# Performance work log

Measured on AMD Instinct MI355X. Metric: run time of the kernel, lower is better.

Reference implementation:

```python
import jax, jax.numpy as jnp
import numpy as np

N = 100000
E = 1600000
D_IN = 128
D_H = 128


def setup_inputs() -> dict:
    key = jax.random.key(0)
    ks = jax.random.split(key, 8)
    x = jax.random.normal(ks[0], (N, D_IN), dtype=jnp.float32)
    edge_index = jax.random.randint(ks[1], (2, E), 0, N, dtype=jnp.int64)
    edge_weights = jax.random.uniform(ks[2], (E,), dtype=jnp.float32)
    # GCNConv params (glorot-ish scale), bias zeros like PyG default init reset
    W1 = jax.random.normal(ks[3], (D_IN, D_H), dtype=jnp.float32) / np.sqrt(D_IN)
    b1 = jnp.zeros((D_H,), dtype=jnp.float32)
    W2 = jax.random.normal(ks[4], (D_H, D_H), dtype=jnp.float32) / np.sqrt(D_H)
    b2 = jnp.zeros((D_H,), dtype=jnp.float32)
    a_prelu = jnp.full((D_H,), 0.25, dtype=jnp.float32)  # nn.PReLU(hidden_dim)
    return {"x": x, "edge_index": edge_index, "edge_weights": edge_weights,
            "W1": W1, "b1": b1, "W2": W2, "b2": b2, "a_prelu": a_prelu}


def _gcn_norm(edge_index, edge_weights, n_nodes):
    # add self loops (weight 1), symmetric normalization deg^-1/2 A deg^-1/2
    loop = jnp.arange(n_nodes, dtype=edge_index.dtype)
    src = jnp.concatenate([edge_index[0], loop])
    dst = jnp.concatenate([edge_index[1], loop])
    w = jnp.concatenate([edge_weights, jnp.ones((n_nodes,), edge_weights.dtype)])
    deg = jax.ops.segment_sum(w, dst, num_segments=n_nodes)
    dis = jnp.where(deg > 0, jax.lax.rsqrt(jnp.maximum(deg, 1e-12)), 0.0)
    norm = dis[src] * w * dis[dst]
    return src, dst, norm


def _gcn_layer(h, W, b, src, dst, norm, n_nodes):
    h = h @ W                                   # [N, D] linear (no bias)
    msg = h[src] * norm[:, None]                # gather + scale  [E+N, D]
    out = jax.ops.segment_sum(msg, dst, num_segments=n_nodes)
    return out + b


def _prelu(z, a):
    return jnp.where(z >= 0, z, a * z)


def reference(x, edge_index, edge_weights, W1, b1, W2, b2, a_prelu):
    n = x.shape[0]
    src, dst, norm = _gcn_norm(edge_index, edge_weights, n)
    z = _prelu(_gcn_layer(x, W1, b1, src, dst, norm, n), a_prelu)
    z = _prelu(_gcn_layer(z, W2, b2, src, dst, norm, n), a_prelu)
    return z
```

## Files before the change

kernel.cpp:

```cpp
#include <hip/hip_runtime.h>
#include <hip/hip_fp16.h>

#define D 128
#define CAP 64
#define NBKT 512
#define CHUNK 4096
#define BKTCAP 5120

typedef _Float16 f16x8 __attribute__((ext_vector_type(8)));
typedef float f32x4 __attribute__((ext_vector_type(4)));

__global__ __launch_bounds__(256) void k_bin(const int* __restrict__ ei,
        const float* __restrict__ ew, int* __restrict__ gcur,
        int2* __restrict__ gbkt, int e, int nbin,
        const float* __restrict__ W1, const float* __restrict__ W2,
        __half* __restrict__ Wpk1, __half* __restrict__ Wpk2) {
    if (blockIdx.x >= nbin) {
        int gidx = (blockIdx.x - nbin) * 256 + threadIdx.x;
        if (gidx >= 4096) return;
        const float* W = (gidx < 2048) ? W1 : W2;
        __half* P = (gidx < 2048) ? Wpk1 : Wpk2;
        int idx = gidx & 2047;
        int lane = idx & 63, nt = (idx >> 6) & 7, ks = idx >> 9;
        int col = nt * 16 + (lane & 15);
        int kb = ks * 32 + (lane >> 4) * 8;
        #pragma unroll
        for (int j = 0; j < 8; ++j)
            P[idx * 8 + j] = __float2half(W[(kb + j) * D + col]);
        return;
    }
    __shared__ int hist[NBKT];
    __shared__ int base[NBKT];
    int t = threadIdx.x;
    int b0 = blockIdx.x * CHUNK;
    int cnt = min(CHUNK, e - b0);
    for (int i = t; i < NBKT; i += 256) hist[i] = 0;
    __syncthreads();
    int meta[16]; float w[16]; int pos[16]; int bkt[16];
    #pragma unroll
    for (int j = 0; j < 16; ++j) {
        int li = t + j * 256;
        bkt[j] = -1;
        if (li < cnt) {
            int i = b0 + li;
            int d = ei[e + i];
            int s = ei[i];
            bkt[j] = d >> 8;
            meta[j] = s | ((d & 255) << 24);
            w[j] = ew[i];
            pos[j] = atomicAdd(&hist[bkt[j]], 1);
        }
    }
    __syncthreads();
    for (int i = t; i < NBKT; i += 256)
        if (hist[i] > 0) base[i] = atomicAdd(&gcur[i], hist[i]);
    __syncthreads();
    #pragma unroll
    for (int j = 0; j < 16; ++j) {
        if (bkt[j] >= 0) {
            int idx = base[bkt[j]] + pos[j];
            if (idx < BKTCAP)
                gbkt[(size_t)bkt[j] * BKTCAP + idx] =
                    make_int2(meta[j], __float_as_int(w[j]));
        }
    }
}

__global__ __launch_bounds__(1024) void k_scat2(const int2* __restrict__ gbkt,
        const int* __restrict__ gcur, const float2* __restrict__ X,
        int2* __restrict__ slot, int* __restrict__ rsc, float* __restrict__ dis,
        __half2* __restrict__ xh, int n) {
    __shared__ int cur[256];
    __shared__ float wsum[256];
    __shared__ float disv[256];
    int bkt = blockIdx.x;
    int nodebase = bkt << 8;
    int t = threadIdx.x;
    int cnt = min(gcur[bkt], BKTCAP);
    if (t < 256) { cur[t] = 0; wsum[t] = 0.f; }
    __syncthreads();
    for (int i = t; i < cnt; i += 1024) {
        int2 r = gbkt[(size_t)bkt * BKTCAP + i];
        int dl = (unsigned)r.x >> 24;
        int pos = atomicAdd(&cur[dl], 1);
        atomicAdd(&wsum[dl], __int_as_float(r.y));
        if (pos < CAP)
            slot[(((size_t)(nodebase + dl)) << 6) + pos] =
                make_int2(r.x & 0xFFFFFF, r.y);
    }
    __syncthreads();
    if (t < 256) {
        int v = nodebase + t;
        float dv = 1.f;
        if (v < n) {
            dv = rsqrtf(1.0f + wsum[t]);
            dis[v] = dv;
            rsc[v] = cur[t];
        }
        disv[t] = dv;
    }
    __syncthreads();
    int nrow = min(256, n - nodebase);
    size_t rowbase = (size_t)nodebase << 6;
    for (int idx = t; idx < nrow * 64; idx += 1024) {
        float dv2 = disv[idx >> 6];
        float2 f = X[rowbase + idx];
        xh[rowbase + idx] = __floats2half2_rn(dv2 * f.x, dv2 * f.y);
    }
}

template <int NU>
__device__ __forceinline__ void aggbatch(int j0, int eslot, int dg, int voff,
        float wf, const char* __restrict__ Hc, float (&acc)[8]) {
    int vo[NU]; float w[NU];
    #pragma unroll
    for (int u = 0; u < NU; ++u) {
        int sl = j0 + 4 * u + eslot;
        vo[u] = __shfl(voff, sl);
        w[u] = __shfl(wf, sl);
    }
    f16x8 g[NU];
    #pragma unroll
    for (int u = 0; u < NU; ++u)
        g[u] = *(const f16x8*)(Hc + vo[u] + (dg << 4));
    #pragma unroll
    for (int u = 0; u < NU; ++u) {
        #pragma unroll
        for (int d = 0; d < 8; ++d)
            acc[d] = fmaf(w[u], (float)g[u][d], acc[d]);
    }
}

__global__ __launch_bounds__(256) void k_agg(const __half2* __restrict__ Hs,
        const int2* __restrict__ slot, const int* __restrict__ rsc,
        const float* __restrict__ dis, __half2* __restrict__ out, int n) {
    int wid = threadIdx.x >> 6, lane = threadIdx.x & 63;
    int v = blockIdx.x * 4 + wid;
    if (v >= n) return;
    int eslot = lane >> 4;
    int dg = lane & 15;
    int c = min(rsc[v], 62);
    int c1 = c + 1;
    const int2* row = slot + ((size_t)v << 6);
    const char* Hc = (const char*)Hs;

    int2 mm;
    if (lane == 0) mm = make_int2(v, 0x3f800000);
    else if (lane < c1) mm = row[lane - 1];
    else mm = make_int2(v, 0);
    int voff = mm.x << 8;
    float wf = __int_as_float(mm.y);

    float acc[8];
    #pragma unroll
    for (int d = 0; d < 8; ++d) acc[d] = 0.f;

    int j0 = 0;
    for (; j0 + 16 <= c1; j0 += 16) aggbatch<4>(j0, eslot, dg, voff, wf, Hc, acc);
    for (; j0 < c1; j0 += 8)        aggbatch<2>(j0, eslot, dg, voff, wf, Hc, acc);

    #pragma unroll
    for (int d = 0; d < 8; ++d) {
        acc[d] += __shfl_xor(acc[d], 16);
        acc[d] += __shfl_xor(acc[d], 32);
    }
    if (eslot == 0) {
        float dv = dis[v];
        union { f16x8 v8; __half2 h[4]; } o;
        #pragma unroll
        for (int d = 0; d < 4; ++d)
            o.h[d] = __floats2half2_rn(dv * acc[2 * d], dv * acc[2 * d + 1]);
        *(f16x8*)((char*)out + ((size_t)v << 8) + (dg << 4)) = o.v8;
    }
}

template <bool HALF_OUT>
__global__ __launch_bounds__(256) void k_gemm(const __half* __restrict__ A,
        const __half* __restrict__ Wpk, const float* __restrict__ b,
        const float* __restrict__ ap, const float* __restrict__ dis,
        void* __restrict__ Cv, int n) {
    int t = threadIdx.x;
    int wv = t >> 6, lane = t & 63;
    int base = blockIdx.x * 64 + wv * 16;
    int row = base + (lane & 15);
    int rowc = min(row, n - 1);
    int kg = lane >> 4;

    const f16x8* Arow = (const f16x8*)(A + (size_t)rowc * D);
    f16x8 afr[4];
    #pragma unroll
    for (int ks = 0; ks < 4; ++ks) afr[ks] = Arow[ks * 4 + kg];

    const f16x8* Wp = (const f16x8*)Wpk;
    f32x4 acc[8];
    #pragma unroll
    for (int nt = 0; nt < 8; ++nt) acc[nt] = (f32x4){0.f, 0.f, 0.f, 0.f};

    #pragma unroll
    for (int ks = 0; ks < 4; ++ks) {
        #pragma unroll
        for (int nt = 0; nt < 8; ++nt) {
            f16x8 bfr = Wp[(ks * 8 + nt) * 64 + lane];
            acc[nt] = __builtin_amdgcn_mfma_f32_16x16x32_f16(afr[ks], bfr, acc[nt], 0, 0, 0);
        }
    }

    int c0 = lane & 15;
    int r0 = base + (lane >> 4) * 4;
    float dv[4];
    #pragma unroll
    for (int q = 0; q < 4; ++q)
        dv[q] = HALF_OUT ? dis[min(r0 + q, n - 1)] : 1.0f;
    #pragma unroll
    for (int nt = 0; nt < 8; ++nt) {
        int col = nt * 16 + c0;
        float bb = b[col], aa = ap[col];
        #pragma unroll
        for (int q = 0; q < 4; ++q) {
            int r = r0 + q;
            if (r < n) {
                float z = acc[nt][q] + bb;
                z = (z >= 0.f) ? z : aa * z;
                if (HALF_OUT) ((__half*)Cv)[(size_t)r * D + col] = __float2half(dv[q] * z);
                else          ((float*)Cv)[(size_t)r * D + col] = z;
            }
        }
    }
}


extern "C" void kernel_launch(void* const* d_in, const int* in_sizes, int n_in,
                              void* d_out, int out_size, void* d_ws, size_t ws_size,
                              hipStream_t stream) {
    const float* x  = (const float*)d_in[0];
    const int*   ei = (const int*)d_in[1];
    const float* ew = (const float*)d_in[2];
    const float* W1 = (const float*)d_in[3];
    const float* b1 = (const float*)d_in[4];
    const float* W2 = (const float*)d_in[5];
    const float* b2 = (const float*)d_in[6];
    const float* ap = (const float*)d_in[7];

    int n = in_sizes[0] / D;
    int e = in_sizes[2];

    int*     gcur = (int*)d_ws;
    float*   dis  = (float*)(gcur + NBKT);
    int*     rsc  = (int*)(dis + n);
    int2*    gbkt = (int2*)(rsc + n);
    int2*    slot = gbkt + (size_t)NBKT * BKTCAP;
    __half2* xh   = (__half2*)(slot + (size_t)n * CAP);
    __half2* z1h  = xh + (size_t)n * 64;
    __half2* ah   = z1h + (size_t)n * 64;
    __half*  Wpk1 = (__half*)(ah + (size_t)n * 64);
    __half*  Wpk2 = Wpk1 + 16384;
    float*   out  = (float*)d_out;

    int nbin = (e + CHUNK - 1) / CHUNK;
    int nbb  = (n + 255) / 256;
    int nbw  = (n + 3) / 4;
    int nbg  = (n + 63) / 64;

    hipMemsetAsync(gcur, 0, NBKT * sizeof(int), stream);
    k_bin<<<nbin + 16, 256, 0, stream>>>(ei, ew, gcur, gbkt, e, nbin, W1, W2, Wpk1, Wpk2);
    k_scat2<<<nbb, 1024, 0, stream>>>(gbkt, gcur, (const float2*)x, slot, rsc, dis, xh, n);

    k_agg<<<nbw, 256, 0, stream>>>(xh, slot, rsc, dis, ah, n);
    k_gemm<true><<<nbg, 256, 0, stream>>>((const __half*)ah, Wpk1, b1, ap, dis, (void*)z1h, n);
    k_agg<<<nbw, 256, 0, stream>>>(z1h, slot, rsc, dis, ah, n);
    k_gemm<false><<<nbg, 256, 0, stream>>>((const __half*)ah, Wpk2, b2, ap, dis, (void*)out, n);
}
```

Measured before the change: 226.1 us.

## Slice feature matrices into column panels and pack edge metadata into 32 bits

Intermediate half-precision feature matrices are stored as four 32-column slices, each holding 64 bytes per node. The aggregation kernel is split so each block processes one slice for two node groups, with 16 edges in flight per wave and 4 lanes per row. Edge slots now pack a 17-bit source index and an fp16 weight into one int, which halves metadata traffic. The aim is to make the gathered working set per slice small enough to stay in cache. The cost is fp16 edge weights, a limit of 131072 nodes, and four times as many aggregation blocks each reading the slot rows.

```diff
diff --git a/kernel.cpp b/kernel.cpp
--- a/kernel.cpp
+++ b/kernel.cpp
@@ -68,8 +68,8 @@
 
 __global__ __launch_bounds__(1024) void k_scat2(const int2* __restrict__ gbkt,
         const int* __restrict__ gcur, const float2* __restrict__ X,
-        int2* __restrict__ slot, int* __restrict__ rsc, float* __restrict__ dis,
-        __half2* __restrict__ xh, int n) {
+        int* __restrict__ mslot, int* __restrict__ rsc, float* __restrict__ dis,
+        __half* __restrict__ xh, int n) {
     __shared__ int cur[256];
     __shared__ float wsum[256];
     __shared__ float disv[256];
@@ -83,10 +83,13 @@
         int2 r = gbkt[(size_t)bkt * BKTCAP + i];
         int dl = (unsigned)r.x >> 24;
         int pos = atomicAdd(&cur[dl], 1);
-        atomicAdd(&wsum[dl], __int_as_float(r.y));
-        if (pos < CAP)
-            slot[(((size_t)(nodebase + dl)) << 6) + pos] =
-                make_int2(r.x & 0xFFFFFF, r.y);
+        float w = __int_as_float(r.y);
+        atomicAdd(&wsum[dl], w);
+        if (pos < CAP) {
+            unsigned hb = (unsigned)__half_as_ushort(__float2half(w));
+            mslot[(((size_t)(nodebase + dl)) << 6) + pos] =
+                (r.x & 0x1FFFF) | (int)(hb << 17);
+        }
     }
     __syncthreads();
     if (t < 256) {
@@ -100,77 +103,65 @@
         disv[t] = dv;
     }
     __syncthreads();
+    size_t n32 = (size_t)n * 32;
     int nrow = min(256, n - nodebase);
-    size_t rowbase = (size_t)nodebase << 6;
     for (int idx = t; idx < nrow * 64; idx += 1024) {
-        float dv2 = disv[idx >> 6];
-        float2 f = X[rowbase + idx];
-        xh[rowbase + idx] = __floats2half2_rn(dv2 * f.x, dv2 * f.y);
-    }
-}
-
-template <int NU>
-__device__ __forceinline__ void aggbatch(int j0, int eslot, int dg, int voff,
-        float wf, const char* __restrict__ Hc, float (&acc)[8]) {
-    int vo[NU]; float w[NU];
-    #pragma unroll
-    for (int u = 0; u < NU; ++u) {
-        int sl = j0 + 4 * u + eslot;
-        vo[u] = __shfl(voff, sl);
-        w[u] = __shfl(wf, sl);
-    }
-    f16x8 g[NU];
-    #pragma unroll
-    for (int u = 0; u < NU; ++u)
-        g[u] = *(const f16x8*)(Hc + vo[u] + (dg << 4));
-    #pragma unroll
-    for (int u = 0; u < NU; ++u) {
-        #pragma unroll
-        for (int d = 0; d < 8; ++d)
-            acc[d] = fmaf(w[u], (float)g[u][d], acc[d]);
-    }
-}
-
-__global__ __launch_bounds__(256) void k_agg(const __half2* __restrict__ Hs,
-        const int2* __restrict__ slot, const int* __restrict__ rsc,
-        const float* __restrict__ dis, __half2* __restrict__ out, int n) {
+        int r = idx >> 6, dp = idx & 63;
+        int grow = nodebase + r;
+        float dv2 = disv[r];
+        float2 f = X[((size_t)grow << 6) + dp];
+        __half2 h = __floats2half2_rn(dv2 * f.x, dv2 * f.y);
+        *(__half2*)(xh + (size_t)(dp >> 4) * n32 + (size_t)grow * 32 + ((dp & 15) << 1)) = h;
+    }
+}
+
+__global__ __launch_bounds__(256) void k_agg(const __half* __restrict__ Hs,
+        const int* __restrict__ mslot, const int* __restrict__ rsc,
+        const float* __restrict__ dis, __half* __restrict__ outp, int n) {
+    int sub = blockIdx.x & 7;
+    int slice = sub >> 1;
+    int nodeblock = (blockIdx.x >> 3) * 2 + (sub & 1);
     int wid = threadIdx.x >> 6, lane = threadIdx.x & 63;
-    int v = blockIdx.x * 4 + wid;
+    int v = nodeblock * 4 + wid;
     if (v >= n) return;
-    int eslot = lane >> 4;
-    int dg = lane & 15;
+    int eg = lane >> 2;
+    int quad = lane & 3;
     int c = min(rsc[v], 62);
     int c1 = c + 1;
-    const int2* row = slot + ((size_t)v << 6);
-    const char* Hc = (const char*)Hs;
-
-    int2 mm;
-    if (lane == 0) mm = make_int2(v, 0x3f800000);
-    else if (lane < c1) mm = row[lane - 1];
-    else mm = make_int2(v, 0);
-    int voff = mm.x << 8;
-    float wf = __int_as_float(mm.y);
+    const int* mrow = mslot + ((size_t)v << 6);
+
+    int mm;
+    if (lane == 0) mm = v | (int)(0x3C00u << 17);
+    else if (lane < c1) mm = mrow[lane - 1];
+    else mm = v;
+
+    size_t n32 = (size_t)n * 32;
+    const char* Hb = (const char*)(Hs + (size_t)slice * n32);
 
     float acc[8];
     #pragma unroll
     for (int d = 0; d < 8; ++d) acc[d] = 0.f;
 
-    int j0 = 0;
-    for (; j0 + 16 <= c1; j0 += 16) aggbatch<4>(j0, eslot, dg, voff, wf, Hc, acc);
-    for (; j0 < c1; j0 += 8)        aggbatch<2>(j0, eslot, dg, voff, wf, Hc, acc);
-
-    #pragma unroll
-    for (int d = 0; d < 8; ++d) {
-        acc[d] += __shfl_xor(acc[d], 16);
-        acc[d] += __shfl_xor(acc[d], 32);
-    }
-    if (eslot == 0) {
+    for (int j0 = 0; j0 < c1; j0 += 16) {
+        int mv = __shfl(mm, j0 + eg);
+        int src = mv & 0x1FFFF;
+        float w = __half2float(__ushort_as_half((unsigned short)((unsigned)mv >> 17)));
+        f16x8 g = *(const f16x8*)(Hb + ((size_t)src << 6) + (quad << 4));
+        #pragma unroll
+        for (int d = 0; d < 8; ++d) acc[d] = fmaf(w, (float)g[d], acc[d]);
+    }
+    #pragma unroll
+    for (int off = 4; off <= 32; off <<= 1) {
+        #pragma unroll
+        for (int d = 0; d < 8; ++d) acc[d] += __shfl_xor(acc[d], off);
+    }
+    if (eg == 0) {
         float dv = dis[v];
         union { f16x8 v8; __half2 h[4]; } o;
         #pragma unroll
         for (int d = 0; d < 4; ++d)
             o.h[d] = __floats2half2_rn(dv * acc[2 * d], dv * acc[2 * d + 1]);
-        *(f16x8*)((char*)out + ((size_t)v << 8) + (dg << 4)) = o.v8;
+        *(f16x8*)((char*)(outp + (size_t)slice * n32) + ((size_t)v << 6) + (quad << 4)) = o.v8;
     }
 }
 
@@ -185,11 +176,12 @@
     int row = base + (lane & 15);
     int rowc = min(row, n - 1);
     int kg = lane >> 4;
-
-    const f16x8* Arow = (const f16x8*)(A + (size_t)rowc * D);
+    size_t n32 = (size_t)n * 32;
+
     f16x8 afr[4];
     #pragma unroll
-    for (int ks = 0; ks < 4; ++ks) afr[ks] = Arow[ks * 4 + kg];
+    for (int ks = 0; ks < 4; ++ks)
+        afr[ks] = *(const f16x8*)(A + (size_t)ks * n32 + (size_t)rowc * 32 + kg * 8);
 
     const f16x8* Wp = (const f16x8*)Wpk;
     f32x4 acc[8];
@@ -221,8 +213,12 @@
             if (r < n) {
                 float z = acc[nt][q] + bb;
                 z = (z >= 0.f) ? z : aa * z;
-                if (HALF_OUT) ((__half*)Cv)[(size_t)r * D + col] = __float2half(dv[q] * z);
-                else          ((float*)Cv)[(size_t)r * D + col] = z;
+                if (HALF_OUT) {
+                    ((__half*)Cv)[(size_t)(nt >> 1) * n32 + (size_t)r * 32 +
+                                  ((nt & 1) * 16 + c0)] = __float2half(dv[q] * z);
+                } else {
+                    ((float*)Cv)[(size_t)r * D + col] = z;
+                }
             }
         }
     }
@@ -244,29 +240,30 @@
     int n = in_sizes[0] / D;
     int e = in_sizes[2];
 
-    int*     gcur = (int*)d_ws;
-    float*   dis  = (float*)(gcur + NBKT);
-    int*     rsc  = (int*)(dis + n);
-    int2*    gbkt = (int2*)(rsc + n);
-    int2*    slot = gbkt + (size_t)NBKT * BKTCAP;
-    __half2* xh   = (__half2*)(slot + (size_t)n * CAP);
-    __half2* z1h  = xh + (size_t)n * 64;
-    __half2* ah   = z1h + (size_t)n * 64;
-    __half*  Wpk1 = (__half*)(ah + (size_t)n * 64);
-    __half*  Wpk2 = Wpk1 + 16384;
-    float*   out  = (float*)d_out;
+    int*     gcur  = (int*)d_ws;
+    float*   dis   = (float*)(gcur + NBKT);
+    int*     rsc   = (int*)(dis + n);
+    int2*    gbkt  = (int2*)(rsc + n);
+    int*     mslot = (int*)(gbkt + (size_t)NBKT * BKTCAP);
+    __half*  xh    = (__half*)(mslot + (size_t)n * 64);
+    __half*  z1h   = xh + (size_t)n * 128;
+    __half*  ah    = z1h + (size_t)n * 128;
+    __half*  Wpk1  = ah + (size_t)n * 128;
+    __half*  Wpk2  = Wpk1 + 16384;
+    float*   out   = (float*)d_out;
 
     int nbin = (e + CHUNK - 1) / CHUNK;
     int nbb  = (n + 255) / 256;
-    int nbw  = (n + 3) / 4;
+    int NB   = (n + 3) / 4;
+    int nba  = ((NB + 1) / 2) * 8;
     int nbg  = (n + 63) / 64;
 
     hipMemsetAsync(gcur, 0, NBKT * sizeof(int), stream);
     k_bin<<<nbin + 16, 256, 0, stream>>>(ei, ew, gcur, gbkt, e, nbin, W1, W2, Wpk1, Wpk2);
-    k_scat2<<<nbb, 1024, 0, stream>>>(gbkt, gcur, (const float2*)x, slot, rsc, dis, xh, n);
-
-    k_agg<<<nbw, 256, 0, stream>>>(xh, slot, rsc, dis, ah, n);
-    k_gemm<true><<<nbg, 256, 0, stream>>>((const __half*)ah, Wpk1, b1, ap, dis, (void*)z1h, n);
-    k_agg<<<nbw, 256, 0, stream>>>(z1h, slot, rsc, dis, ah, n);
-    k_gemm<false><<<nbg, 256, 0, stream>>>((const __half*)ah, Wpk2, b2, ap, dis, (void*)out, n);
-}
+    k_scat2<<<nbb, 1024, 0, stream>>>(gbkt, gcur, (const float2*)x, mslot, rsc, dis, xh, n);
+
+    k_agg<<<nba, 256, 0, stream>>>(xh, mslot, rsc, dis, ah, n);
+    k_gemm<true><<<nbg, 256, 0, stream>>>(ah, Wpk1, b1, ap, dis, (void*)z1h, n);
+    k_agg<<<nba, 256, 0, stream>>>(z1h, mslot, rsc, dis, ah, n);
+    k_gemm<false><<<nbg, 256, 0, stream>>>(ah, Wpk2, b2, ap, dis, (void*)out, n);
+}
```

After: 389.0 us. +72.0%, slower.
